# Optimization experiments

Measured on AMD Instinct MI355X. Metric: run time of the kernel, lower is better.

The kernel has to match this reference:

```python
import jax, jax.numpy as jnp
import numpy as np

N = 131072          # total nodes per batched graph side
E = 524288          # total edges per batched graph side (avg degree 4)
B = 4096            # number of graph pairs
NPG = 32            # nodes per graph
NEG_SLOPE = 0.2
LN_EPS = 1e-5


def setup_inputs() -> dict:
    key = jax.random.key(0)
    ks = jax.random.split(key, 40)
    rn = lambda k, s, sc=0.05: jax.random.normal(k, s, dtype=jnp.float32) * sc
    inp = {}
    inp["feat1"] = jax.random.normal(ks[0], (N, 6), dtype=jnp.float32)
    inp["feat2"] = jax.random.normal(ks[1], (N, 6), dtype=jnp.float32)
    inp["llm_emb"] = jax.random.normal(ks[2], (B, 1024), dtype=jnp.float32)
    inp["src1"] = jax.random.randint(ks[3], (E,), 0, N, dtype=jnp.int32)
    inp["dst1"] = jax.random.randint(ks[4], (E,), 0, N, dtype=jnp.int32)
    inp["src2"] = jax.random.randint(ks[5], (E,), 0, N, dtype=jnp.int32)
    inp["dst2"] = jax.random.randint(ks[6], (E,), 0, N, dtype=jnp.int32)
    inp["gid"] = (jnp.arange(N, dtype=jnp.int32) // NPG).astype(jnp.int32)
    # shared GAT weights (layer: W[in,H*Dh], attn_l[H,Dh], attn_r[H,Dh], bias[H*Dh])
    inp["W1"] = rn(ks[7], (6, 128));   inp["al1"] = rn(ks[8], (4, 32));  inp["ar1"] = rn(ks[9], (4, 32));  inp["b1"] = rn(ks[10], (128,))
    inp["W2"] = rn(ks[11], (128, 128)); inp["al2"] = rn(ks[12], (4, 32)); inp["ar2"] = rn(ks[13], (4, 32)); inp["b2"] = rn(ks[14], (128,))
    inp["W3"] = rn(ks[15], (128, 256)); inp["al3"] = rn(ks[16], (4, 64)); inp["ar3"] = rn(ks[17], (4, 64)); inp["b3"] = rn(ks[18], (256,))
    # fusion
    inp["Wpg"] = rn(ks[19], (512, 512)); inp["bpg"] = rn(ks[20], (512,))
    inp["Wpl"] = rn(ks[21], (1024, 512)); inp["bpl"] = rn(ks[22], (512,))
    inp["Wv"] = rn(ks[23], (512, 512));  inp["bv"] = rn(ks[24], (512,))
    inp["Wo"] = rn(ks[25], (512, 512));  inp["bo"] = rn(ks[26], (512,))
    inp["gamma"] = jnp.ones((512,), jnp.float32); inp["beta"] = jnp.zeros((512,), jnp.float32)
    # classifier
    inp["Wc1"] = rn(ks[27], (512, 256)); inp["bc1"] = rn(ks[28], (256,))
    inp["Wc2"] = rn(ks[29], (256, 1));   inp["bc2"] = rn(ks[30], (1,))
    return inp


def _gat(x, src, dst, W, al, ar, b):
    # DGL GATConv: e_ij = LeakyReLU(a_l.h_src + a_r.h_dst), softmax over edges per dst
    H, Dh = al.shape
    h = (x @ W).reshape(-1, H, Dh)                 # [N,H,Dh]
    el = jnp.sum(h * al, axis=-1)                  # [N,H]
    er = jnp.sum(h * ar, axis=-1)                  # [N,H]
    e = jax.nn.leaky_relu(el[src] + er[dst], NEG_SLOPE)   # [E,H]
    m = jax.ops.segment_max(e, dst, num_segments=N)
    a = jnp.exp(e - m[dst])
    s = jax.ops.segment_sum(a, dst, num_segments=N)
    alpha = a / jnp.where(s[dst] == 0, 1.0, s[dst])       # [E,H]
    out = jax.ops.segment_sum(alpha[:, :, None] * h[src], dst, num_segments=N)
    return out.reshape(-1, H * Dh) + b


def _gnn(x, src, dst, gid, W1, al1, ar1, b1, W2, al2, ar2, b2, W3, al3, ar3, b3):
    h = jax.nn.relu(_gat(x, src, dst, W1, al1, ar1, b1))
    h = jax.nn.relu(_gat(h, src, dst, W2, al2, ar2, b2))
    h = _gat(h, src, dst, W3, al3, ar3, b3)        # [N,256]
    sums = jax.ops.segment_sum(h, gid, num_segments=B)
    cnt = jax.ops.segment_sum(jnp.ones((h.shape[0], 1), h.dtype), gid, num_segments=B)
    return sums / cnt                               # [B,256] mean_nodes


def reference(feat1, feat2, llm_emb, src1, dst1, src2, dst2, gid,
              W1, al1, ar1, b1, W2, al2, ar2, b2, W3, al3, ar3, b3,
              Wpg, bpg, Wpl, bpl, Wv, bv, Wo, bo, gamma, beta,
              Wc1, bc1, Wc2, bc2):
    h1 = _gnn(feat1, src1, dst1, gid, W1, al1, ar1, b1, W2, al2, ar2, b2, W3, al3, ar3, b3)
    h2 = _gnn(feat2, src2, dst2, gid, W1, al1, ar1, b1, W2, al2, ar2, b2, W3, al3, ar3, b3)
    pair = jnp.concatenate([h1, h2], axis=1)        # [B,512]
    gp = pair @ Wpg + bpg                           # [B,512]
    lp = llm_emb @ Wpl + bpl                        # [B,512]
    # MHA with kv seq_len 1: softmax over a single key == 1 -> out = W_o(W_v gp)
    attn = (gp @ Wv + bv) @ Wo + bo
    x = attn + lp
    mu = jnp.mean(x, axis=-1, keepdims=True)
    var = jnp.mean((x - mu) ** 2, axis=-1, keepdims=True)
    fused = (x - mu) / jnp.sqrt(var + LN_EPS) * gamma + beta
    hcls = jax.nn.relu(fused @ Wc1 + bc1)
    return jax.nn.sigmoid(hcls @ Wc2 + bc2)         # [B,1]
```

## Files before the change

### kernel.cpp

```cpp
#include <hip/hip_runtime.h>
#include <hip/hip_fp8.h>

#define NN 131072
#define NE 524288
#define NB 4096
#define CAP 16
#define NEG_SLOPE 0.2f
#define LN_EPS 1e-5f

typedef unsigned short bf16;
typedef __attribute__((ext_vector_type(8))) short short8;
typedef __attribute__((ext_vector_type(4))) float floatx4;
typedef __attribute__((ext_vector_type(2))) float floatx2;

__device__ __forceinline__ float bf2f(bf16 h) {
    return __uint_as_float((unsigned)h << 16);
}
__device__ __forceinline__ bf16 f2bf(float f) {
    unsigned u = __float_as_uint(f);
    unsigned r = (u + 0x7FFFu + ((u >> 16) & 1u)) >> 16;
    return (bf16)r;
}
__device__ __forceinline__ unsigned char ftofp8(float f) {
    return (unsigned char)(__builtin_amdgcn_cvt_pk_fp8_f32(f, f, 0, false) & 0xFF);
}
__device__ __forceinline__ float leaky(float x) {
    return fmaxf(x, 0.f) + NEG_SLOPE * fminf(x, 0.f);
}


__global__ void zero_i32(int* p, int n) {
    int i = blockIdx.x * blockDim.x + threadIdx.x;
    if (i < n) p[i] = 0;
}

__global__ void scatter_slots_kernel(const int* __restrict__ s0, const int* __restrict__ d0,
                                     const int* __restrict__ s1, const int* __restrict__ d1,
                                     int* __restrict__ deg, int* __restrict__ slots) {
    int i = blockIdx.x * blockDim.x + threadIdx.x;
    int side = i >= NE;
    int e = i - side * NE;
    int d = side ? d1[e] : d0[e];
    int s = side ? s1[e] : s0[e];
    int gd = side * NN + d;
    int p = atomicAdd(&deg[gd], 1);
    if (p < CAP) slots[(size_t)gd * CAP + p] = side * NN + s;
}

#define PREP_TOTAL (16384 + 32768 + 524288 + 131072 + 2048 + 2048 + 48)

__global__ void prep_all_kernel(const float* __restrict__ W2, const float* __restrict__ W3,
                                const float* __restrict__ Wpl, const float* __restrict__ Wc1,
                                const float* __restrict__ W1,
                                const float* __restrict__ al1, const float* __restrict__ ar1,
                                const float* __restrict__ al2, const float* __restrict__ ar2,
                                const float* __restrict__ al3, const float* __restrict__ ar3,
                                bf16* __restrict__ W2t, bf16* __restrict__ W3t,
                                bf16* __restrict__ Wplt, bf16* __restrict__ Wc1t,
                                bf16* __restrict__ Ff2, bf16* __restrict__ Ff3,
                                float* __restrict__ F1) {
    int i = blockIdx.x * blockDim.x + threadIdx.x;
    if (i < 16384) {
        int c = i >> 7, k = i & 127;
        W2t[i] = f2bf(W2[k * 128 + c]);
        return;
    }
    i -= 16384;
    if (i < 32768) {
        int c = i >> 7, k = i & 127;
        W3t[i] = f2bf(W3[k * 256 + c]);
        return;
    }
    i -= 32768;
    if (i < 524288) {
        int c = i >> 10, k = i & 1023;
        Wplt[i] = f2bf(Wpl[k * 512 + c]);
        return;
    }
    i -= 524288;
    if (i < 131072) {
        int c = i >> 9, k = i & 511;
        Wc1t[i] = f2bf(Wc1[k * 256 + c]);
        return;
    }
    i -= 131072;
    if (i < 2048) {
        int c = i >> 7, k = i & 127;
        float s = 0.f;
        if (c < 8) {
            const float* a = (c < 4) ? al2 : ar2;
            int hh = c & 3;
            for (int d = 0; d < 32; d++) s += W2[k * 128 + hh * 32 + d] * a[hh * 32 + d];
        }
        Ff2[i] = f2bf(s);
        return;
    }
    i -= 2048;
    if (i < 2048) {
        int c = i >> 7, k = i & 127;
        float s = 0.f;
        if (c < 8) {
            const float* a = (c < 4) ? al3 : ar3;
            int hh = c & 3;
            for (int d = 0; d < 64; d++) s += W3[k * 256 + hh * 64 + d] * a[hh * 64 + d];
        }
        Ff3[i] = f2bf(s);
        return;
    }
    i -= 2048;
    if (i < 48) {
        int k = i >> 3, c = i & 7;
        const float* a = (c < 4) ? al1 : ar1;
        int hh = c & 3;
        float s = 0.f;
        for (int d = 0; d < 32; d++) s += W1[k * 128 + hh * 32 + d] * a[hh * 32 + d];
        F1[k * 8 + c] = s;
    }
}

__global__ void f2bf_kernel(const float* __restrict__ x, bf16* __restrict__ y) {
    int i = blockIdx.x * blockDim.x + threadIdx.x;
    float4 v = ((const float4*)x)[i];
    ushort4 u;
    u.x = f2bf(v.x); u.y = f2bf(v.y); u.z = f2bf(v.z); u.w = f2bf(v.w);
    ((ushort4*)y)[i] = u;
}

__global__ void wt_kernel(const float* __restrict__ W, bf16* __restrict__ Wt, int K, int C) {
    int i = blockIdx.x * blockDim.x + threadIdx.x;
    if (i >= K * C) return;
    int c = i / K, k = i - c * K;
    Wt[i] = f2bf(W[(size_t)k * C + c]);
}


__global__ void elr1_kernel(const float* __restrict__ f0, const float* __restrict__ f1,
                            const float* __restrict__ F1,
                            float* __restrict__ el, float* __restrict__ er) {
    int n = blockIdx.x * blockDim.x + threadIdx.x;
    const float* x = (n < NN) ? (f0 + (size_t)n * 6) : (f1 + (size_t)(n - NN) * 6);
    float xv[6];
#pragma unroll
    for (int k = 0; k < 6; k++) xv[k] = x[k];
#pragma unroll
    for (int c = 0; c < 4; c++) {
        float sl = 0.f, sr = 0.f;
#pragma unroll
        for (int k = 0; k < 6; k++) {
            sl += xv[k] * F1[k * 8 + c];
            sr += xv[k] * F1[k * 8 + c + 4];
        }
        el[n * 4 + c] = sl;
        er[n * 4 + c] = sr;
    }
}

__global__ __launch_bounds__(256) void agg1lin_kernel(
        const float* __restrict__ f0, const float* __restrict__ f1,
        const float* __restrict__ el, const float* __restrict__ er,
        const int* __restrict__ deg, const int* __restrict__ slots,
        const float* __restrict__ W1, const float* __restrict__ b1,
        bf16* __restrict__ xb) {
    __shared__ float sagg[8][32];
    int node0 = blockIdx.x * 8;
    int grp = threadIdx.x >> 5;
    int gl = threadIdx.x & 31;
    int wid = node0 + grp;
    int head = gl >> 3, dim = gl & 7;
    int dg = deg[wid];
    dg = (dg > CAP) ? CAP : dg;
    float erh = er[wid * 4 + head];
    const int* sp = slots + (size_t)wid * CAP;
    float acc = 0.f, ssum = 0.f;
    bool live = dim < 6;
    for (int p = 0; p < dg; p += 4) {
        int4 s4 = *(const int4*)(sp + p);
        int s[4]; bool v[4];
        s[0] = s4.x; v[0] = true;
        v[1] = p + 1 < dg; s[1] = v[1] ? s4.y : s4.x;
        v[2] = p + 2 < dg; s[2] = v[2] ? s4.z : s4.x;
        v[3] = p + 3 < dg; s[3] = v[3] ? s4.w : s4.x;
        float elv[4], xv[4];
#pragma unroll
        for (int k = 0; k < 4; k++) {
            int g = s[k];
            elv[k] = el[g * 4 + head];
            const float* fp = (g < NN) ? (f0 + (size_t)g * 6) : (f1 + (size_t)(g - NN) * 6);
            xv[k] = live ? fp[dim] : 0.f;
        }
#pragma unroll
        for (int k = 0; k < 4; k++) {
            float w = v[k] ? __expf(leaky(elv[k] + erh)) : 0.f;
            ssum += w;
            acc += w * xv[k];
        }
    }
    float rs = (dg > 0) ? 1.f / ssum : 0.f;
    sagg[grp][gl] = acc * rs;
    __syncthreads();
    int o = threadIdx.x * 4;
    int n2 = o >> 7, cbase = o & 127;
    int hd = cbase >> 5;
    const float* ax = &sagg[n2][hd * 8];
    float a0 = ax[0], a1 = ax[1], a2 = ax[2], a3 = ax[3], a4 = ax[4], a5 = ax[5];
    ushort4 uo;
    unsigned short* up = (unsigned short*)&uo;
#pragma unroll
    for (int j = 0; j < 4; j++) {
        int c = cbase + j;
        float a = b1[c];
        a += a0 * W1[0 * 128 + c]; a += a1 * W1[1 * 128 + c];
        a += a2 * W1[2 * 128 + c]; a += a3 * W1[3 * 128 + c];
        a += a4 * W1[4 * 128 + c]; a += a5 * W1[5 * 128 + c];
        up[j] = f2bf(fmaxf(a, 0.f));
    }
    *(ushort4*)(xb + (size_t)(node0 + n2) * 128 + cbase) = uo;
}

__device__ __forceinline__ void softmax_phaseA(const float* __restrict__ el,
                                               const float* __restrict__ er,
                                               const int* __restrict__ slots,
                                               int wid, int dg, int lane,
                                               float* alpha_out, int* src_out) {
    int e = lane & 15, h = lane >> 4;
    int sA = slots[(size_t)wid * CAP + e];
    int sAc = (e < dg) ? sA : 0;
    float erh = er[wid * 4 + h];
    float elv = el[sAc * 4 + h];
    float w = (e < dg) ? __expf(leaky(elv + erh)) : 0.f;
    float ssum = w;
    ssum += __shfl_xor(ssum, 1, 64);
    ssum += __shfl_xor(ssum, 2, 64);
    ssum += __shfl_xor(ssum, 4, 64);
    ssum += __shfl_xor(ssum, 8, 64);
    *alpha_out = (dg > 0) ? w * (1.f / ssum) : 0.f;
    *src_out = sAc;
}

__global__ void agg2_kernel(const unsigned char* __restrict__ h8, const float* __restrict__ el,
                            const float* __restrict__ er, const int* __restrict__ deg,
                            const int* __restrict__ slots, const float* __restrict__ bias,
                            bf16* __restrict__ out) {
    int t = blockIdx.x * blockDim.x + threadIdx.x;
    int wid = t >> 5;
    int gl = threadIdx.x & 31;
    int dg = deg[wid];
    dg = (dg > CAP) ? CAP : dg;
    int head = gl >> 3;
    int fbase = gl * 4;
    float erh = er[wid * 4 + head];
    const int* sp = slots + (size_t)wid * CAP;
    float a0 = 0.f, a1 = 0.f, a2 = 0.f, a3 = 0.f, ssum = 0.f;

    for (int p = 0; p < dg; p += 4) {
        int4 s4 = *(const int4*)(sp + p);
        int s[4]; bool v[4];
        s[0] = s4.x; v[0] = true;
        v[1] = p + 1 < dg; s[1] = v[1] ? s4.y : s4.x;
        v[2] = p + 2 < dg; s[2] = v[2] ? s4.z : s4.x;
        v[3] = p + 3 < dg; s[3] = v[3] ? s4.w : s4.x;
        float elv[4]; unsigned u1[4];
#pragma unroll
        for (int k = 0; k < 4; k++) {
            elv[k] = el[s[k] * 4 + head];
            u1[k] = *(const unsigned*)(h8 + (size_t)s[k] * 128 + fbase);
        }
#pragma unroll
        for (int k = 0; k < 4; k++) {
            float w = v[k] ? __expf(leaky(elv[k] + erh)) : 0.f;
            ssum += w;
            floatx2 lo = __builtin_amdgcn_cvt_pk_f32_fp8((int)u1[k], false);
            floatx2 hi = __builtin_amdgcn_cvt_pk_f32_fp8((int)u1[k], true);
            a0 += w * lo[0]; a1 += w * lo[1];
            a2 += w * hi[0]; a3 += w * hi[1];
        }
    }
    float rs = (dg > 0) ? 1.f / ssum : 0.f;
    float4 bbv = *(const float4*)(bias + fbase);
    float v0 = fmaxf(a0 * rs + bbv.x, 0.f), v1 = fmaxf(a1 * rs + bbv.y, 0.f);
    float v2 = fmaxf(a2 * rs + bbv.z, 0.f), v3 = fmaxf(a3 * rs + bbv.w, 0.f);
    uint2 uo;
    uo.x = (unsigned)f2bf(v0) | ((unsigned)f2bf(v1) << 16);
    uo.y = (unsigned)f2bf(v2) | ((unsigned)f2bf(v3) << 16);
    *(uint2*)(out + (size_t)wid * 128 + fbase) = uo;
}

__global__ void agg3pool_kernel(const unsigned char* __restrict__ h8,
                                const float* __restrict__ el, const float* __restrict__ er,
                                const int* __restrict__ deg, const int* __restrict__ slots,
                                const float* __restrict__ bias, bf16* __restrict__ pair) {
    __shared__ float red[4 * 256];
    int side = blockIdx.x >> 12;
    int b = blockIdx.x & 4095;
    int nodebase = side * NN + b * 32;
    int grp = threadIdx.x >> 6, lane = threadIdx.x & 63;
    int fbase = lane * 4;
    int grpbase = lane & 48;
    float p0 = 0.f, p1 = 0.f, p2 = 0.f, p3 = 0.f;

    for (int nn = 0; nn < 8; nn++) {
        int wid = nodebase + grp * 8 + nn;
        int dg = deg[wid];
        dg = (dg > CAP) ? CAP : dg;
        float alpha; int sAc;
        softmax_phaseA(el, er, slots, wid, dg, lane, &alpha, &sAc);
        for (int p = 0; p < dg; p += 4) {
            int sc[4]; float av[4];
#pragma unroll
            for (int k = 0; k < 4; k++) {
                int srcl = grpbase + p + k;
                sc[k] = __shfl(sAc, srcl, 64);
                av[k] = __shfl(alpha, srcl, 64);
            }
            unsigned u[4];
#pragma unroll
            for (int k = 0; k < 4; k++)
                u[k] = *(const unsigned*)(h8 + (size_t)sc[k] * 256 + fbase);
#pragma unroll
            for (int k = 0; k < 4; k++) {
                floatx2 lo = __builtin_amdgcn_cvt_pk_f32_fp8((int)u[k], false);
                floatx2 hi = __builtin_amdgcn_cvt_pk_f32_fp8((int)u[k], true);
                p0 += av[k] * lo[0]; p1 += av[k] * lo[1];
                p2 += av[k] * hi[0]; p3 += av[k] * hi[1];
            }
        }
    }
    red[grp * 256 + fbase + 0] = p0;
    red[grp * 256 + fbase + 1] = p1;
    red[grp * 256 + fbase + 2] = p2;
    red[grp * 256 + fbase + 3] = p3;
    __syncthreads();
    if (grp == 0) {
        float4 bbv = *(const float4*)(bias + fbase);
        float s0 = 0.f, s1 = 0.f, s2 = 0.f, s3 = 0.f;
#pragma unroll
        for (int g = 0; g < 4; g++) {
            s0 += red[g * 256 + fbase + 0];
            s1 += red[g * 256 + fbase + 1];
            s2 += red[g * 256 + fbase + 2];
            s3 += red[g * 256 + fbase + 3];
        }
        const float inv = 1.0f / 32.0f;
        float v0 = s0 * inv + bbv.x, v1 = s1 * inv + bbv.y;
        float v2 = s2 * inv + bbv.z, v3 = s3 * inv + bbv.w;
        uint2 uo;
        uo.x = (unsigned)f2bf(v0) | ((unsigned)f2bf(v1) << 16);
        uo.y = (unsigned)f2bf(v2) | ((unsigned)f2bf(v3) << 16);
        *(uint2*)(pair + (size_t)b * 512 + side * 256 + fbase) = uo;
    }
}

template <bool FOLD, bool OUT8>
__global__ __launch_bounds__(256) void mgemm_kernel(const bf16* __restrict__ A,
                                                    const bf16* __restrict__ Wt,
                                                    const float* __restrict__ bias,
                                                    void* __restrict__ out,
                                                    int K, int C, int relu,
                                                    const bf16* __restrict__ Ff,
                                                    float* __restrict__ el,
                                                    float* __restrict__ er) {
    __shared__ short As[128 * 48];
    __shared__ short Bs[128 * 48];
    int t = threadIdx.x;
    int wave = t >> 6, lane = t & 63;
    int wm = (wave >> 1) * 64, wn = (wave & 1) * 64;
    int bm = blockIdx.x * 128, bn = blockIdx.y * 128;
    int m_lane = lane & 15, quad = lane >> 4;
    bool dofold = FOLD && (blockIdx.y == 0) && (wn == 0);

    floatx4 acc[4][4];
#pragma unroll
    for (int i = 0; i < 4; i++)
#pragma unroll
        for (int j = 0; j < 4; j++) acc[i][j] = (floatx4){0.f, 0.f, 0.f, 0.f};
    floatx4 facc[4];
    if (FOLD) {
#pragma unroll
        for (int i = 0; i < 4; i++) facc[i] = (floatx4){0.f, 0.f, 0.f, 0.f};
    }

    int lrow = t >> 2, lq = t & 3;
    for (int k0 = 0; k0 < K; k0 += 32) {
        __syncthreads();
#pragma unroll
        for (int pass = 0; pass < 2; pass++) {
            int row = lrow + pass * 64;
            *(short8*)&As[row * 48 + lq * 8] =
                *(const short8*)(A + (size_t)(bm + row) * K + k0 + lq * 8);
            *(short8*)&Bs[row * 48 + lq * 8] =
                *(const short8*)(Wt + (size_t)(bn + row) * K + k0 + lq * 8);
        }
        __syncthreads();
        short8 af[4], bf[4];
#pragma unroll
        for (int i = 0; i < 4; i++)
            af[i] = *(const short8*)&As[(wm + i * 16 + m_lane) * 48 + quad * 8];
#pragma unroll
        for (int j = 0; j < 4; j++)
            bf[j] = *(const short8*)&Bs[(wn + j * 16 + m_lane) * 48 + quad * 8];
        if (dofold) {
            short8 fbv = *(const short8*)(Ff + m_lane * K + k0 + quad * 8);
#pragma unroll
            for (int i = 0; i < 4; i++)
                facc[i] = __builtin_amdgcn_mfma_f32_16x16x32_bf16(af[i], fbv, facc[i], 0, 0, 0);
        }
#pragma unroll
        for (int i = 0; i < 4; i++)
#pragma unroll
            for (int j = 0; j < 4; j++)
                acc[i][j] = __builtin_amdgcn_mfma_f32_16x16x32_bf16(af[i], bf[j], acc[i][j], 0, 0, 0);
    }

#pragma unroll
    for (int i = 0; i < 4; i++) {
#pragma unroll
        for (int j = 0; j < 4; j++) {
            int gc = bn + wn + j * 16 + m_lane;
            float bbv = bias ? bias[gc] : 0.f;
#pragma unroll
            for (int r = 0; r < 4; r++) {
                int gr = bm + wm + i * 16 + quad * 4 + r;
                float v = acc[i][j][r] + bbv;
                if (relu) v = fmaxf(v, 0.f);
                if (OUT8) ((unsigned char*)out)[(size_t)gr * C + gc] = ftofp8(v);
                else      ((bf16*)out)[(size_t)gr * C + gc] = f2bf(v);
            }
        }
    }
    if (dofold && m_lane < 8) {
        float* dst = (m_lane < 4) ? el : er;
        int hh = m_lane & 3;
#pragma unroll
        for (int i = 0; i < 4; i++)
#pragma unroll
            for (int r = 0; r < 4; r++) {
                int gr = bm + wm + i * 16 + quad * 4 + r;
                dst[gr * 4 + hh] = facc[i][r];
            }
    }
}

__global__ __launch_bounds__(256) void fgemm512_kernel(const float* __restrict__ A,
                                                       const float* __restrict__ B,
                                                       float* __restrict__ C) {
    const int BK = 16;
    __shared__ float As[BK][68];
    __shared__ float Bs[BK][68];
    int t = threadIdx.x;
    int bm = blockIdx.x * 64, bn = blockIdx.y * 64;
    int tm0 = (t & 15) * 4, tn0 = (t >> 4) * 4;
    float acc[4][4] = {};
    int la_m = t >> 2, la_k = (t & 3) * 4;
    int lb_k = t >> 4, lb_c = (t & 15) * 4;

    for (int k0 = 0; k0 < 512; k0 += BK) {
        float4 a4 = *(const float4*)(A + (size_t)(bm + la_m) * 512 + k0 + la_k);
        float4 b4 = *(const float4*)(B + (size_t)(k0 + lb_k) * 512 + bn + lb_c);
        As[la_k + 0][la_m] = a4.x; As[la_k + 1][la_m] = a4.y;
        As[la_k + 2][la_m] = a4.z; As[la_k + 3][la_m] = a4.w;
        *(float4*)&Bs[lb_k][lb_c] = b4;
        __syncthreads();
#pragma unroll
        for (int k = 0; k < BK; k++) {
            float4 av = *(const float4*)&As[k][tm0];
            float4 bv = *(const float4*)&Bs[k][tn0];
            acc[0][0] += av.x * bv.x; acc[0][1] += av.x * bv.y; acc[0][2] += av.x * bv.z; acc[0][3] += av.x * bv.w;
            acc[1][0] += av.y * bv.x; acc[1][1] += av.y * bv.y; acc[1][2] += av.y * bv.z; acc[1][3] += av.y * bv.w;
            acc[2][0] += av.z * bv.x; acc[2][1] += av.z * bv.y; acc[2][2] += av.z * bv.z; acc[2][3] += av.z * bv.w;
            acc[3][0] += av.w * bv.x; acc[3][1] += av.w * bv.y; acc[3][2] += av.w * bv.z; acc[3][3] += av.w * bv.w;
        }
        __syncthreads();
    }
#pragma unroll
    for (int i = 0; i < 4; i++) {
        float4 o = make_float4(acc[i][0], acc[i][1], acc[i][2], acc[i][3]);
        *(float4*)(C + (size_t)(bm + tm0 + i) * 512 + bn + tn0) = o;
    }
}

__global__ void biasstep_kernel(const float* __restrict__ vin, const float* __restrict__ M,
                                const float* __restrict__ badd, float* __restrict__ vout) {
    int c = blockIdx.x * blockDim.x + threadIdx.x;
    float s = 0.f;
    for (int k = 0; k < 512; k++) s += vin[k] * M[(size_t)k * 512 + c];
    vout[c] = s + badd[c];
}


__global__ void ln_kernel(const bf16* __restrict__ attn, const bf16* __restrict__ lp,
                          const float* __restrict__ gamma, const float* __restrict__ beta,
                          bf16* __restrict__ out) {
    __shared__ float red[256];
    int b = blockIdx.x, t = threadIdx.x;
    size_t base = (size_t)b * 512;
    float x0 = bf2f(attn[base + t]) + bf2f(lp[base + t]);
    float x1 = bf2f(attn[base + 256 + t]) + bf2f(lp[base + 256 + t]);
    red[t] = x0 + x1; __syncthreads();
    for (int off = 128; off > 0; off >>= 1) { if (t < off) red[t] += red[t + off]; __syncthreads(); }
    float mu = red[0] * (1.0f / 512.0f);
    __syncthreads();
    float d0 = x0 - mu, d1 = x1 - mu;
    red[t] = d0 * d0 + d1 * d1; __syncthreads();
    for (int off = 128; off > 0; off >>= 1) { if (t < off) red[t] += red[t + off]; __syncthreads(); }
    float rstd = rsqrtf(red[0] * (1.0f / 512.0f) + LN_EPS);
    out[base + t]       = f2bf(d0 * rstd * gamma[t] + beta[t]);
    out[base + 256 + t] = f2bf(d1 * rstd * gamma[256 + t] + beta[256 + t]);
}

__global__ void cls2_kernel(const bf16* __restrict__ hc, const float* __restrict__ Wc2,
                            const float* __restrict__ bc2, float* __restrict__ out) {
    int wid = (blockIdx.x * blockDim.x + threadIdx.x) >> 6;
    int lane = threadIdx.x & 63;
    if (wid >= NB) return;
    float s = 0.f;
#pragma unroll
    for (int j = 0; j < 4; j++) {
        int k = lane + 64 * j;
        s += bf2f(hc[(size_t)wid * 256 + k]) * Wc2[k];
    }
    for (int off = 32; off > 0; off >>= 1) s += __shfl_down(s, off);
    if (lane == 0) {
        float v = s + bc2[0];
        out[wid] = 1.0f / (1.0f + __expf(-v));
    }
}


static inline size_t alup(size_t x) { return (x + 255) & ~(size_t)255; }

extern "C" void kernel_launch(void* const* d_in, const int* in_sizes, int n_in,
                              void* d_out, int out_size, void* d_ws, size_t ws_size,
                              hipStream_t stream) {
    const float* feat0 = (const float*)d_in[0];
    const float* feat1 = (const float*)d_in[1];
    const float* llm = (const float*)d_in[2];
    const int* srcs[2] = {(const int*)d_in[3], (const int*)d_in[5]};
    const int* dsts[2] = {(const int*)d_in[4], (const int*)d_in[6]};
    const float* W1 = (const float*)d_in[8];
    const float* al[3] = {(const float*)d_in[9],  (const float*)d_in[13], (const float*)d_in[17]};
    const float* ar[3] = {(const float*)d_in[10], (const float*)d_in[14], (const float*)d_in[18]};
    const float* bb[3] = {(const float*)d_in[11], (const float*)d_in[15], (const float*)d_in[19]};
    const float* W2 = (const float*)d_in[12];
    const float* W3 = (const float*)d_in[16];
    const float* Wpg = (const float*)d_in[20]; const float* bpg = (const float*)d_in[21];
    const float* Wpl = (const float*)d_in[22]; const float* bpl = (const float*)d_in[23];
    const float* Wv  = (const float*)d_in[24]; const float* bv  = (const float*)d_in[25];
    const float* Wo  = (const float*)d_in[26]; const float* bo  = (const float*)d_in[27];
    const float* gamma = (const float*)d_in[28]; const float* beta = (const float*)d_in[29];
    const float* Wc1 = (const float*)d_in[30]; const float* bc1 = (const float*)d_in[31];
    const float* Wc2 = (const float*)d_in[32]; const float* bc2 = (const float*)d_in[33];
    float* outp = (float*)d_out;

    const size_t N2 = (size_t)2 * NN;

    char* p = (char*)d_ws;
    auto take = [&](size_t bytes) { char* r = p; p += alup(bytes); return r; };
    bf16*  xb     = (bf16*)take(N2 * 128 * 2);
    char*  regB   = (char*)take(N2 * 256);
    float* el     = (float*)take(N2 * 4 * 4);
    float* er     = (float*)take(N2 * 4 * 4);
    int*   deg    = (int*)take(N2 * 4);
    int*   slots  = (int*)take(N2 * CAP * 4);
    bf16*  pair   = (bf16*)take((size_t)NB * 512 * 2);
    bf16*  llm_bf = (bf16*)take((size_t)NB * 1024 * 2);
    bf16*  W2t  = (bf16*)take(128 * 128 * 2);
    bf16*  W3t  = (bf16*)take(128 * 256 * 2);
    bf16*  Wplt = (bf16*)take(1024 * 512 * 2);
    bf16*  Wc1t = (bf16*)take(512 * 256 * 2);
    bf16*  Wcot = (bf16*)take(512 * 512 * 2);
    float* F1   = (float*)take(6 * 8 * 4);
    bf16*  Ff2  = (bf16*)take(16 * 128 * 2);
    bf16*  Ff3  = (bf16*)take(16 * 128 * 2);
    float* c1   = (float*)take(512 * 512 * 4);
    float* c2   = (float*)take(512 * 512 * 4);
    float* bias1 = (float*)take(512 * 4);
    float* bco   = (float*)take(512 * 4);
    unsigned char* hb2  = (unsigned char*)regB;
    unsigned char* hb3  = (unsigned char*)regB;
    bf16* fbb   = (bf16*)regB;
    bf16* lp    = fbb + (size_t)0 * NB * 512;
    bf16* attn  = fbb + (size_t)1 * NB * 512;
    bf16* fused = fbb + (size_t)2 * NB * 512;
    bf16* hc    = fbb + (size_t)3 * NB * 512;
    (void)ws_size; (void)n_in; (void)in_sizes; (void)out_size;

    auto mgemm = [&](const bf16* A, const bf16* Wt, const float* bias, bf16* o,
                     int M, int K, int C, int relu) {
        dim3 g(M / 128, C / 128);
        mgemm_kernel<false, false><<<g, 256, 0, stream>>>(A, Wt, bias, o, K, C, relu,
                                                          nullptr, nullptr, nullptr);
    };

    prep_all_kernel<<<(PREP_TOTAL + 255) / 256, 256, 0, stream>>>(
        W2, W3, Wpl, Wc1, W1, al[0], ar[0], al[1], ar[1], al[2], ar[2],
        W2t, W3t, Wplt, Wc1t, Ff2, Ff3, F1);
    f2bf_kernel<<<NB * 1024 / 4 / 256, 256, 0, stream>>>(llm, llm_bf);
    {
        dim3 g8(8, 8);
        fgemm512_kernel<<<g8, 256, 0, stream>>>(Wpg, Wv, c1);
        fgemm512_kernel<<<g8, 256, 0, stream>>>(c1, Wo, c2);
        wt_kernel<<<(512 * 512 + 255) / 256, 256, 0, stream>>>(c2, Wcot, 512, 512);
        biasstep_kernel<<<2, 256, 0, stream>>>(bpg, Wv, bv, bias1);
        biasstep_kernel<<<2, 256, 0, stream>>>(bias1, Wo, bo, bco);
    }

    zero_i32<<<2 * NN / 256, 256, 0, stream>>>(deg, 2 * NN);
    scatter_slots_kernel<<<2 * NE / 256, 256, 0, stream>>>(srcs[0], dsts[0],
                                                           srcs[1], dsts[1], deg, slots);

    elr1_kernel<<<2 * NN / 256, 256, 0, stream>>>(feat0, feat1, F1, el, er);
    agg1lin_kernel<<<2 * NN / 8, 256, 0, stream>>>(feat0, feat1, el, er, deg, slots,
                                                   W1, bb[0], xb);
    {
        dim3 g(2 * NN / 128, 1);
        mgemm_kernel<true, true><<<g, 256, 0, stream>>>(xb, W2t, nullptr, hb2, 128, 128, 0,
                                                        Ff2, el, er);
    }
    agg2_kernel<<<2 * NN * 32 / 256, 256, 0, stream>>>(hb2, el, er, deg, slots, bb[1], xb);
    {
        dim3 g(2 * NN / 128, 2);
        mgemm_kernel<true, true><<<g, 256, 0, stream>>>(xb, W3t, nullptr, hb3, 128, 256, 0,
                                                        Ff3, el, er);
    }
    agg3pool_kernel<<<2 * NB, 256, 0, stream>>>(hb3, el, er, deg, slots, bb[2], pair);

    mgemm(llm_bf, Wplt, bpl, lp, NB, 1024, 512, 0);
    mgemm(pair, Wcot, bco, attn, NB, 512, 512, 0);
    ln_kernel<<<NB, 256, 0, stream>>>(attn, lp, gamma, beta, fused);
    mgemm(fused, Wc1t, bc1, hc, NB, 512, 256, 1);
    cls2_kernel<<<NB / 4, 256, 0, stream>>>(hc, Wc2, bc2, outp);
}
```

Before: 667.1 us.

## Rewrite layer-1 GAT aggregation as thread-per-node with MFMA linear projection

Layer-1 aggregation now assigns one thread per destination node and handles all four heads at once, reading 8-float padded features and float4 attention logits. The old per-lane scalar W1 projection is replaced by an MFMA bf16 GEMM against a block-diagonal W1 matrix with the bias folded in through a constant-one column. Attention logits are prescaled by log2(e) so exp2 can be used, and bf16 packing uses a hardware convert instruction. This is meant to cut scalar FLOPs, redundant gathers and launch count, at the cost of bf16 rounding of the aggregated features and higher register use.

```diff
diff --git a/kernel.cpp b/kernel.cpp
--- a/kernel.cpp
+++ b/kernel.cpp
@@ -7,12 +7,19 @@
 #define CAP 16
 #define NEG_SLOPE 0.2f
 #define LN_EPS 1e-5f
+#define LOG2E 1.44269504088896f
 
 typedef unsigned short bf16;
 typedef __attribute__((ext_vector_type(8))) short short8;
 typedef __attribute__((ext_vector_type(4))) float floatx4;
 typedef __attribute__((ext_vector_type(2))) float floatx2;
 
+#if __has_builtin(__builtin_amdgcn_exp2f)
+#define EXP2(x) __builtin_amdgcn_exp2f(x)
+#else
+#define EXP2(x) exp2f(x)
+#endif
+
 __device__ __forceinline__ float bf2f(bf16 h) {
     return __uint_as_float((unsigned)h << 16);
 }
@@ -20,6 +27,11 @@
     unsigned u = __float_as_uint(f);
     unsigned r = (u + 0x7FFFu + ((u >> 16) & 1u)) >> 16;
     return (bf16)r;
+}
+__device__ __forceinline__ unsigned pkbf(float lo, float hi) {
+    unsigned r;
+    asm("v_cvt_pk_bf16_f32 %0, %1, %2" : "=v"(r) : "v"(lo), "v"(hi));
+    return r;
 }
 __device__ __forceinline__ unsigned char ftofp8(float f) {
     return (unsigned char)(__builtin_amdgcn_cvt_pk_fp8_f32(f, f, 0, false) & 0xFF);
@@ -47,7 +59,7 @@
     if (p < CAP) slots[(size_t)gd * CAP + p] = side * NN + s;
 }
 
-#define PREP_TOTAL (16384 + 32768 + 524288 + 131072 + 2048 + 2048 + 48)
+#define PREP_TOTAL (16384 + 32768 + 524288 + 131072 + 2048 + 2048 + 48 + 4096)
 
 __global__ void prep_all_kernel(const float* __restrict__ W2, const float* __restrict__ W3,
                                 const float* __restrict__ Wpl, const float* __restrict__ Wc1,
@@ -55,10 +67,11 @@
                                 const float* __restrict__ al1, const float* __restrict__ ar1,
                                 const float* __restrict__ al2, const float* __restrict__ ar2,
                                 const float* __restrict__ al3, const float* __restrict__ ar3,
+                                const float* __restrict__ b1v,
                                 bf16* __restrict__ W2t, bf16* __restrict__ W3t,
                                 bf16* __restrict__ Wplt, bf16* __restrict__ Wc1t,
                                 bf16* __restrict__ Ff2, bf16* __restrict__ Ff3,
-                                float* __restrict__ F1) {
+                                float* __restrict__ F1, bf16* __restrict__ W1f) {
     int i = blockIdx.x * blockDim.x + threadIdx.x;
     if (i < 16384) {
         int c = i >> 7, k = i & 127;
@@ -114,7 +127,19 @@
         int hh = c & 3;
         float s = 0.f;
         for (int d = 0; d < 32; d++) s += W1[k * 128 + hh * 32 + d] * a[hh * 32 + d];
-        F1[k * 8 + c] = s;
+        F1[k * 8 + c] = s * LOG2E;
+        return;
+    }
+    i -= 48;
+    if (i < 4096) {
+        int c = i >> 5, k = i & 31;
+        int h = c >> 5, d = k & 7;
+        float v = 0.f;
+        if ((k >> 3) == h) {
+            if (d < 6) v = W1[d * 128 + c];
+            else if (d == 6) v = b1v[c];
+        }
+        W1f[i] = f2bf(v);
     }
 }
 
@@ -134,14 +159,20 @@
 }
 
 
-__global__ void elr1_kernel(const float* __restrict__ f0, const float* __restrict__ f1,
-                            const float* __restrict__ F1,
-                            float* __restrict__ el, float* __restrict__ er) {
+__global__ void featelr_kernel(const float* __restrict__ f0, const float* __restrict__ f1,
+                               const float* __restrict__ F1, float* __restrict__ fpk,
+                               float* __restrict__ el, float* __restrict__ er) {
     int n = blockIdx.x * blockDim.x + threadIdx.x;
     const float* x = (n < NN) ? (f0 + (size_t)n * 6) : (f1 + (size_t)(n - NN) * 6);
     float xv[6];
 #pragma unroll
     for (int k = 0; k < 6; k++) xv[k] = x[k];
+    float4* o = (float4*)(fpk + (size_t)n * 8);
+    o[0] = make_float4(xv[0], xv[1], xv[2], xv[3]);
+    o[1] = make_float4(xv[4], xv[5], 0.f, 0.f);
+    float4 elv, erv;
+    float* ep = (float*)&elv;
+    float* rp = (float*)&erv;
 #pragma unroll
     for (int c = 0; c < 4; c++) {
         float sl = 0.f, sr = 0.f;
@@ -150,72 +181,98 @@
             sl += xv[k] * F1[k * 8 + c];
             sr += xv[k] * F1[k * 8 + c + 4];
         }
-        el[n * 4 + c] = sl;
-        er[n * 4 + c] = sr;
-    }
-}
-
-__global__ __launch_bounds__(256) void agg1lin_kernel(
-        const float* __restrict__ f0, const float* __restrict__ f1,
-        const float* __restrict__ el, const float* __restrict__ er,
-        const int* __restrict__ deg, const int* __restrict__ slots,
-        const float* __restrict__ W1, const float* __restrict__ b1,
+        ep[c] = sl;
+        rp[c] = sr;
+    }
+    *(float4*)(el + (size_t)n * 4) = elv;
+    *(float4*)(er + (size_t)n * 4) = erv;
+}
+
+__global__ __launch_bounds__(256) void agg1mfma_kernel(
+        const float* __restrict__ fpk, const float* __restrict__ el,
+        const float* __restrict__ er, const int* __restrict__ deg,
+        const int* __restrict__ slots, const bf16* __restrict__ W1fg,
         bf16* __restrict__ xb) {
-    __shared__ float sagg[8][32];
-    int node0 = blockIdx.x * 8;
-    int grp = threadIdx.x >> 5;
-    int gl = threadIdx.x & 31;
-    int wid = node0 + grp;
-    int head = gl >> 3, dim = gl & 7;
-    int dg = deg[wid];
+    __shared__ bf16 sW[128 * 40];
+    __shared__ bf16 sagg[256 * 40];
+    int t = threadIdx.x;
+    if (t < 128) {
+        const uint4* src = (const uint4*)(W1fg + t * 32);
+        uint4* dstp = (uint4*)(sW + t * 40);
+        dstp[0] = src[0]; dstp[1] = src[1]; dstp[2] = src[2]; dstp[3] = src[3];
+    }
+
+    int node = blockIdx.x * 256 + t;
+    int dg = deg[node];
     dg = (dg > CAP) ? CAP : dg;
-    float erh = er[wid * 4 + head];
-    const int* sp = slots + (size_t)wid * CAP;
-    float acc = 0.f, ssum = 0.f;
-    bool live = dim < 6;
+    float4 er4 = *(const float4*)(er + (size_t)node * 4);
+    const int* sp = slots + (size_t)node * CAP;
+    float a0[4], a1[4], a2[4], a3[4], a4[4], a5[4], ss[4];
+#pragma unroll
+    for (int h = 0; h < 4; h++) {
+        a0[h] = a1[h] = a2[h] = a3[h] = a4[h] = a5[h] = ss[h] = 0.f;
+    }
     for (int p = 0; p < dg; p += 4) {
         int4 s4 = *(const int4*)(sp + p);
-        int s[4]; bool v[4];
-        s[0] = s4.x; v[0] = true;
-        v[1] = p + 1 < dg; s[1] = v[1] ? s4.y : s4.x;
-        v[2] = p + 2 < dg; s[2] = v[2] ? s4.z : s4.x;
-        v[3] = p + 3 < dg; s[3] = v[3] ? s4.w : s4.x;
-        float elv[4], xv[4];
+        int sarr[4] = {s4.x, s4.y, s4.z, s4.w};
 #pragma unroll
         for (int k = 0; k < 4; k++) {
-            int g = s[k];
-            elv[k] = el[g * 4 + head];
-            const float* fp = (g < NN) ? (f0 + (size_t)g * 6) : (f1 + (size_t)(g - NN) * 6);
-            xv[k] = live ? fp[dim] : 0.f;
-        }
-#pragma unroll
-        for (int k = 0; k < 4; k++) {
-            float w = v[k] ? __expf(leaky(elv[k] + erh)) : 0.f;
-            ssum += w;
-            acc += w * xv[k];
-        }
-    }
-    float rs = (dg > 0) ? 1.f / ssum : 0.f;
-    sagg[grp][gl] = acc * rs;
+            bool vld = (p + k) < dg;
+            int g = vld ? sarr[k] : s4.x;
+            float4 e4 = *(const float4*)(el + (size_t)g * 4);
+            float4 xa = *(const float4*)(fpk + (size_t)g * 8);
+            float4 xc = *(const float4*)(fpk + (size_t)g * 8 + 4);
+            float eh[4] = {e4.x, e4.y, e4.z, e4.w};
+            float rh[4] = {er4.x, er4.y, er4.z, er4.w};
+#pragma unroll
+            for (int h = 0; h < 4; h++) {
+                float z = eh[h] + rh[h];
+                float w = EXP2(fmaxf(z, 0.f) + NEG_SLOPE * fminf(z, 0.f));
+                w = vld ? w : 0.f;
+                ss[h] += w;
+                a0[h] += w * xa.x; a1[h] += w * xa.y; a2[h] += w * xa.z;
+                a3[h] += w * xa.w; a4[h] += w * xc.x; a5[h] += w * xc.y;
+            }
+        }
+    }
+#pragma unroll
+    for (int h = 0; h < 4; h++) {
+        float rs = (dg > 0) ? 1.f / ss[h] : 0.f;
+        uint4 o;
+        o.x = pkbf(a0[h] * rs, a1[h] * rs);
+        o.y = pkbf(a2[h] * rs, a3[h] * rs);
+        o.z = pkbf(a4[h] * rs, a5[h] * rs);
+        o.w = 0x00003F80u;
+        *(uint4*)(sagg + t * 40 + h * 8) = o;
+    }
     __syncthreads();
-    int o = threadIdx.x * 4;
-    int n2 = o >> 7, cbase = o & 127;
-    int hd = cbase >> 5;
-    const float* ax = &sagg[n2][hd * 8];
-    float a0 = ax[0], a1 = ax[1], a2 = ax[2], a3 = ax[3], a4 = ax[4], a5 = ax[5];
-    ushort4 uo;
-    unsigned short* up = (unsigned short*)&uo;
-#pragma unroll
-    for (int j = 0; j < 4; j++) {
-        int c = cbase + j;
-        float a = b1[c];
-        a += a0 * W1[0 * 128 + c]; a += a1 * W1[1 * 128 + c];
-        a += a2 * W1[2 * 128 + c]; a += a3 * W1[3 * 128 + c];
-        a += a4 * W1[4 * 128 + c]; a += a5 * W1[5 * 128 + c];
-        up[j] = f2bf(fmaxf(a, 0.f));
-    }
-    *(ushort4*)(xb + (size_t)(node0 + n2) * 128 + cbase) = uo;
-}
+
+    int wave = t >> 6, lane = t & 63;
+    int mlane = lane & 15, quad = lane >> 4;
+    short8 af[8];
+#pragma unroll
+    for (int j = 0; j < 8; j++)
+        af[j] = *(const short8*)(sW + (j * 16 + mlane) * 40 + quad * 8);
+    floatx4 z4 = (floatx4){0.f, 0.f, 0.f, 0.f};
+#pragma unroll
+    for (int nt = 0; nt < 4; nt++) {
+        int lrow = wave * 64 + nt * 16 + mlane;
+        short8 bfr = *(const short8*)(sagg + lrow * 40 + quad * 8);
+        floatx4 c[8];
+#pragma unroll
+        for (int j = 0; j < 8; j++)
+            c[j] = __builtin_amdgcn_mfma_f32_16x16x32_bf16(af[j], bfr, z4, 0, 0, 0);
+        bf16* op = xb + (size_t)(blockIdx.x * 256 + lrow) * 128 + quad * 4;
+#pragma unroll
+        for (int j = 0; j < 8; j++) {
+            uint2 o;
+            o.x = pkbf(fmaxf(c[j][0], 0.f), fmaxf(c[j][1], 0.f));
+            o.y = pkbf(fmaxf(c[j][2], 0.f), fmaxf(c[j][3], 0.f));
+            *(uint2*)(op + j * 16) = o;
+        }
+    }
+}
+
 
 __device__ __forceinline__ void softmax_phaseA(const float* __restrict__ el,
                                                const float* __restrict__ er,
@@ -571,10 +628,12 @@
     float* F1   = (float*)take(6 * 8 * 4);
     bf16*  Ff2  = (bf16*)take(16 * 128 * 2);
     bf16*  Ff3  = (bf16*)take(16 * 128 * 2);
+    bf16*  W1fg = (bf16*)take(128 * 32 * 2);
     float* c1   = (float*)take(512 * 512 * 4);
     float* c2   = (float*)take(512 * 512 * 4);
     float* bias1 = (float*)take(512 * 4);
     float* bco   = (float*)take(512 * 4);
+    float* fpk          = (float*)regB;
     unsigned char* hb2  = (unsigned char*)regB;
     unsigned char* hb3  = (unsigned char*)regB;
     bf16* fbb   = (bf16*)regB;
@@ -592,8 +651,8 @@
     };
 
     prep_all_kernel<<<(PREP_TOTAL + 255) / 256, 256, 0, stream>>>(
-        W2, W3, Wpl, Wc1, W1, al[0], ar[0], al[1], ar[1], al[2], ar[2],
-        W2t, W3t, Wplt, Wc1t, Ff2, Ff3, F1);
+        W2, W3, Wpl, Wc1, W1, al[0], ar[0], al[1], ar[1], al[2], ar[2], bb[0],
+        W2t, W3t, Wplt, Wc1t, Ff2, Ff3, F1, W1fg);
     f2bf_kernel<<<NB * 1024 / 4 / 256, 256, 0, stream>>>(llm, llm_bf);
     {
         dim3 g8(8, 8);
@@ -608,9 +667,8 @@
     scatter_slots_kernel<<<2 * NE / 256, 256, 0, stream>>>(srcs[0], dsts[0],
                                                            srcs[1], dsts[1], deg, slots);
 
-    elr1_kernel<<<2 * NN / 256, 256, 0, stream>>>(feat0, feat1, F1, el, er);
-    agg1lin_kernel<<<2 * NN / 8, 256, 0, stream>>>(feat0, feat1, el, er, deg, slots,
-                                                   W1, bb[0], xb);
+    featelr_kernel<<<2 * NN / 256, 256, 0, stream>>>(feat0, feat1, F1, fpk, el, er);
+    agg1mfma_kernel<<<2 * NN / 256, 256, 0, stream>>>(fpk, el, er, deg, slots, W1fg, xb);
     {
         dim3 g(2 * NN / 128, 1);
         mgemm_kernel<true, true><<<g, 256, 0, stream>>>(xb, W2t, nullptr, hb2, 128, 128, 0,
```

New measurement: 625.5 us. -6.2%, faster.
